# Kernel tuning notes

Hardware: AMD Instinct MI355X
Metric: run time of the kernel (lower is better)

## Reference

```python
import jax, jax.numpy as jnp
import numpy as np

B, S, D_IN, D_OUT, H = 4, 2048, 1024, 1024, 16
HD = D_OUT // H

def setup_inputs() -> dict:
    key = jax.random.key(0)
    ks = jax.random.split(key, 6)
    s = 1.0 / np.sqrt(D_IN)
    return {
        "x": jax.random.normal(ks[0], (B, S, D_IN), dtype=jnp.float32),
        "Wq": jax.random.uniform(ks[1], (D_IN, D_OUT), jnp.float32, -s, s),
        "Wk": jax.random.uniform(ks[2], (D_IN, D_OUT), jnp.float32, -s, s),
        "Wv": jax.random.uniform(ks[3], (D_IN, D_OUT), jnp.float32, -s, s),
        "Wo": jax.random.uniform(ks[4], (D_OUT, D_OUT), jnp.float32, -s, s),
        "bo": jax.random.uniform(ks[5], (D_OUT,), jnp.float32, -s, s),
    }

def reference(x, Wq, Wk, Wv, Wo, bo):
    b, n, _ = x.shape
    # project and split heads: [b, h, n, hd]
    q = (x @ Wq).reshape(b, n, H, HD).transpose(0, 2, 1, 3)
    k = (x @ Wk).reshape(b, n, H, HD).transpose(0, 2, 1, 3)
    v = (x @ Wv).reshape(b, n, H, HD).transpose(0, 2, 1, 3)
    scores = jnp.einsum("bhqd,bhkd->bhqk", q, k) / np.sqrt(HD).astype(np.float32)
    causal = jnp.tril(jnp.ones((n, n), dtype=bool))
    scores = jnp.where(causal, scores, -jnp.inf)
    attn = jax.nn.softmax(scores, axis=-1)  # dropout p=0.0 -> identity
    ctx = jnp.einsum("bhqk,bhkd->bhqd", attn, v)
    ctx = ctx.transpose(0, 2, 1, 3).reshape(b, n, D_OUT)
    return ctx @ Wo + bo
```

## Files before the change

### kernel.cpp

```cpp
#include <hip/hip_runtime.h>
#include <stdint.h>

#define B_   4
#define S_   2048
#define DI   1024
#define DOUT 1024
#define NHD  16
#define HD   64

typedef __attribute__((ext_vector_type(8))) short short8;
typedef __attribute__((ext_vector_type(4))) float f32x4;
typedef __attribute__((ext_vector_type(16))) float f32x16;

__device__ __forceinline__ unsigned short f32_bf16(float f) {
  union { float f; unsigned u; } v; v.f = f;
  unsigned r = v.u + 0x7FFFu + ((v.u >> 16) & 1u);
  return (unsigned short)(r >> 16);
}

__device__ __forceinline__ unsigned pack_bf16x2(float a, float b) {
  union { float f; unsigned u; } x, y; x.f = a; y.f = b;
  return ((y.u + 0x8000u) & 0xFFFF0000u) | ((x.u + 0x8000u) >> 16);
}

__device__ __forceinline__ void gl_lds16(const void* g, void* s) {
  __builtin_amdgcn_global_load_lds(
      (const __attribute__((address_space(1))) unsigned int*)g,
      (__attribute__((address_space(3))) unsigned int*)s, 16, 0, 0);
}

#define EXP2(x) __builtin_amdgcn_exp2f(x)

__global__ __launch_bounds__(256) void cvt_kernel(const float* __restrict__ src,
                                                  unsigned short* __restrict__ dst, int n4) {
  int i = blockIdx.x * blockDim.x + threadIdx.x;
  if (i < n4) {
    float4 v = ((const float4*)src)[i];
    ushort4 o;
    o.x = f32_bf16(v.x); o.y = f32_bf16(v.y); o.z = f32_bf16(v.z); o.w = f32_bf16(v.w);
    ((ushort4*)dst)[i] = o;
  }
}

__global__ __launch_bounds__(256) void wtrans_kernel(const float* __restrict__ W,
                                                     unsigned short* __restrict__ Wt) {
  __shared__ __attribute__((aligned(16))) float tile[64][65];
  const int k0 = blockIdx.y * 64;
  const int n0 = blockIdx.x * 64;
  const int tid = threadIdx.x;
#pragma unroll
  for (int i = 0; i < 4; i++) {
    int c = tid + i * 256;
    int r = c >> 4;
    int cc = (c & 15) * 4;
    float4 v = *(const float4*)(W + (size_t)(k0 + r) * DOUT + n0 + cc);
    tile[r][cc] = v.x; tile[r][cc + 1] = v.y; tile[r][cc + 2] = v.z; tile[r][cc + 3] = v.w;
  }
  __syncthreads();
#pragma unroll
  for (int i = 0; i < 4; i++) {
    int c = tid + i * 256;
    int r = c >> 4;
    int cc = (c & 15) * 4;
    ushort4 o;
    o.x = f32_bf16(tile[cc + 0][r]);
    o.y = f32_bf16(tile[cc + 1][r]);
    o.z = f32_bf16(tile[cc + 2][r]);
    o.w = f32_bf16(tile[cc + 3][r]);
    *(ushort4*)(Wt + (size_t)(n0 + r) * DI + k0 + cc) = o;
  }
}

__global__ __launch_bounds__(256) void vtrans_kernel(const unsigned short* __restrict__ Vb,
                                                     unsigned short* __restrict__ Vt) {
  __shared__ __attribute__((aligned(16))) unsigned short tile[64][72];
  const int bh = blockIdx.y;
  const int s0 = blockIdx.x * 64;
  const int tid = threadIdx.x;
  const unsigned short* src = Vb + (size_t)bh * S_ * HD + (size_t)s0 * HD;
#pragma unroll
  for (int i = 0; i < 2; i++) {
    int c = tid + i * 256;
    int r = c >> 3;
    int cc = (c & 7) * 8;
    *(uint4*)(&tile[r][cc]) = *(const uint4*)(src + r * HD + cc);
  }
  __syncthreads();
  unsigned short* dst = Vt + (size_t)bh * HD * S_ + s0;
#pragma unroll
  for (int i = 0; i < 2; i++) {
    int c = tid + i * 256;
    int r = c >> 3;
    int cc = (c & 7) * 8;
    union { unsigned short u[8]; uint4 v; } t;
#pragma unroll
    for (int j = 0; j < 8; j++) t.u[j] = tile[cc + j][r];
    *(uint4*)(dst + (size_t)r * S_ + cc) = t.v;
  }
}

template <int MODE>
__global__ __launch_bounds__(256) void gemm_kernel(
    const unsigned short* __restrict__ A,
    const unsigned short* __restrict__ Bt,
    unsigned short* __restrict__ oQ,
    unsigned short* __restrict__ oK,
    unsigned short* __restrict__ oV,
    float* __restrict__ outF,
    const float* __restrict__ bias,
    int M, int N, int K) {
  __shared__ __attribute__((aligned(16))) unsigned short Asm_[128 * 32];
  __shared__ __attribute__((aligned(16))) unsigned short Bsm_[128 * 32];
  const int tid = threadIdx.x;
  const int lane = tid & 63;
  const int w = tid >> 6;
  const int wm = w >> 1, wn = w & 1;
  const int quad = lane >> 4, l16 = lane & 15;
  const int m0 = blockIdx.x * 128;
  const int n0 = blockIdx.y * 128;

  const int lr = lane >> 2;
  const int lc8 = (lane & 3) * 8;
  const unsigned short* gA0 = A + (size_t)(m0 + w * 32 + lr) * K + lc8;
  const unsigned short* gA1 = gA0 + (size_t)16 * K;
  const unsigned short* gB0 = Bt + (size_t)(n0 + w * 32 + lr) * K + lc8;
  const unsigned short* gB1 = gB0 + (size_t)16 * K;
  unsigned short* sA0 = Asm_ + (w * 2 + 0) * 512;
  unsigned short* sA1 = Asm_ + (w * 2 + 1) * 512;
  unsigned short* sB0 = Bsm_ + (w * 2 + 0) * 512;
  unsigned short* sB1 = Bsm_ + (w * 2 + 1) * 512;

  f32x4 acc[4][4] = {};

  for (int k0 = 0; k0 < K; k0 += 32) {
    __syncthreads();
    gl_lds16(gA0 + k0, sA0);
    gl_lds16(gA1 + k0, sA1);
    gl_lds16(gB0 + k0, sB0);
    gl_lds16(gB1 + k0, sB1);
    __syncthreads();
    short8 af[4], bfr[4];
#pragma unroll
    for (int mi = 0; mi < 4; mi++)
      af[mi] = *(const short8*)(Asm_ + (wm * 64 + mi * 16 + l16) * 32 + quad * 8);
#pragma unroll
    for (int ni = 0; ni < 4; ni++)
      bfr[ni] = *(const short8*)(Bsm_ + (wn * 64 + ni * 16 + l16) * 32 + quad * 8);
#pragma unroll
    for (int mi = 0; mi < 4; mi++)
#pragma unroll
      for (int ni = 0; ni < 4; ni++)
        acc[mi][ni] = __builtin_amdgcn_mfma_f32_16x16x32_bf16(af[mi], bfr[ni], acc[mi][ni], 0, 0, 0);
  }

  unsigned short* dst0 = nullptr;
  if (MODE == 0) {
    const int which = n0 >> 10;
    dst0 = which == 0 ? oQ : which == 1 ? oK : oV;
  }
#pragma unroll
  for (int mi = 0; mi < 4; mi++) {
#pragma unroll
    for (int ni = 0; ni < 4; ni++) {
      const int col = n0 + wn * 64 + ni * 16 + l16;
      float bv = (MODE == 1) ? bias[col] : 0.f;
#pragma unroll
      for (int r = 0; r < 4; r++) {
        const int row = m0 + wm * 64 + mi * 16 + quad * 4 + r;
        if (MODE == 0) {
          int b = row >> 11, s = row & 2047;
          int h = (col >> 6) & 15, hd = col & 63;
          dst0[(((size_t)(b * NHD + h)) * S_ + s) * HD + hd] = f32_bf16(acc[mi][ni][r]);
        } else {
          outF[(size_t)row * N + col] = acc[mi][ni][r] + bv;
        }
      }
    }
  }
}

__global__ __launch_bounds__(512, 2) void attn_kernel(
    const unsigned short* __restrict__ Q,
    const unsigned short* __restrict__ Kmat,
    const unsigned short* __restrict__ Vt,
    unsigned short* __restrict__ ctx) {
  __shared__ __attribute__((aligned(16))) unsigned short Ks[2][64 * 64];
  __shared__ __attribute__((aligned(16))) unsigned short Vs[2][64 * 64];
  __shared__ __attribute__((aligned(16))) unsigned short PsT[256 * 72];

  const int tid = threadIdx.x;
  const int lane = tid & 63;
  const int w = tid >> 6;
  const int l32 = lane & 31;
  const int h = lane >> 5;

  const int bh = blockIdx.x & 63;
  const int i4 = blockIdx.x >> 6;
  const int jj = (i4 < 4) ? 7 - i4 : i4 - 4;
  const int qc = jj * 8 + w;
  const int nt = (qc >> 1) + 1;
  const int ntmax = jj * 4 + 4;

  const unsigned short* Qh = Q + (size_t)bh * S_ * HD;
  const unsigned short* Kh = Kmat + (size_t)bh * S_ * HD;
  const unsigned short* Vh = Vt + (size_t)bh * HD * S_;

  const int qrow = qc * 32 + l32;

  short8 qf[4];
#pragma unroll
  for (int ks = 0; ks < 4; ks++)
    qf[ks] = *(const short8*)(Qh + (size_t)qrow * HD + ks * 16 + h * 8);

  const int sr = tid >> 3;
  const int sj = tid & 7;
  const int ssw = sr * 64 + ((sj ^ (sr & 7)) << 3);
  const unsigned short* gK = Kh + (size_t)sr * HD + sj * 8;
  const unsigned short* gV = Vh + (size_t)sr * S_ + sj * 8;
  const int swz = (l32 & 7);

  uint4 kreg = *(const uint4*)(gK);
  uint4 vreg = *(const uint4*)(gV);
  *(uint4*)(&Ks[0][ssw]) = kreg;
  *(uint4*)(&Vs[0][ssw]) = vreg;
  __syncthreads();

  f32x16 oacc[2] = {};
  float m_run = -__builtin_inff();
  float l_run = 0.f;
  unsigned short* myP = PsT + (size_t)(w * 32) * 72;
  const float scl = 0.18033688f;

  for (int kt = 0; kt < ntmax; kt++) {
    if (kt + 1 < ntmax) {
      kreg = *(const uint4*)(gK + (size_t)(kt + 1) * 64 * HD);
      vreg = *(const uint4*)(gV + (size_t)(kt + 1) * 64);
    }
    const unsigned short* Kb_ = Ks[kt & 1];
    const unsigned short* Vb_ = Vs[kt & 1];

    if (kt < nt) {
      const int k0 = kt * 64;
      f32x16 sacc[2] = {};
#pragma unroll
      for (int ks = 0; ks < 4; ks++)
#pragma unroll
        for (int mi = 0; mi < 2; mi++) {
          short8 kf = *(const short8*)(Kb_ + (mi * 32 + l32) * 64 + (((ks * 2 + h) ^ swz) << 3));
          sacc[mi] = __builtin_amdgcn_mfma_f32_32x32x16_bf16(kf, qf[ks], sacc[mi], 0, 0, 0);
        }

      if (kt == nt - 1) {
#pragma unroll
        for (int mi = 0; mi < 2; mi++)
#pragma unroll
          for (int e = 0; e < 16; e++) {
            int key = k0 + mi * 32 + (e & 3) + 8 * (e >> 2) + 4 * h;
            if (key > qrow) sacc[mi][e] = -__builtin_inff();
          }
      }
      float vmax = -__builtin_inff();
#pragma unroll
      for (int mi = 0; mi < 2; mi++)
#pragma unroll
        for (int e = 0; e < 16; e++) vmax = fmaxf(vmax, sacc[mi][e]);
      vmax = fmaxf(vmax, __shfl_xor(vmax, 32));
      const float mnew = fmaxf(m_run, vmax * scl);
      const float alpha = EXP2(m_run - mnew);
      m_run = mnew;

      float rs = 0.f;
#pragma unroll
      for (int mi = 0; mi < 2; mi++)
#pragma unroll
        for (int e = 0; e < 16; e++) {
          float p = EXP2(fmaf(sacc[mi][e], scl, -mnew));
          sacc[mi][e] = p;
          rs += p;
        }
      rs += __shfl_xor(rs, 32);
      l_run = l_run * alpha + rs;
#pragma unroll
      for (int mi = 0; mi < 2; mi++) oacc[mi] *= alpha;

#pragma unroll
      for (int mi = 0; mi < 2; mi++)
#pragma unroll
        for (int g = 0; g < 4; g++) {
          uint2 pk;
          pk.x = pack_bf16x2(sacc[mi][4 * g + 0], sacc[mi][4 * g + 1]);
          pk.y = pack_bf16x2(sacc[mi][4 * g + 2], sacc[mi][4 * g + 3]);
          *(uint2*)(myP + l32 * 72 + mi * 32 + g * 8 + h * 4) = pk;
        }

#pragma unroll
      for (int ks2 = 0; ks2 < 4; ks2++) {
        short8 pf = *(const short8*)(myP + l32 * 72 + ks2 * 16 + h * 8);
#pragma unroll
        for (int mi2 = 0; mi2 < 2; mi2++) {
          short8 vf = *(const short8*)(Vb_ + (mi2 * 32 + l32) * 64 + (((ks2 * 2 + h) ^ swz) << 3));
          oacc[mi2] = __builtin_amdgcn_mfma_f32_32x32x16_bf16(vf, pf, oacc[mi2], 0, 0, 0);
        }
      }
    }

    if (kt + 1 < ntmax) {
      *(uint4*)(&Ks[(kt + 1) & 1][ssw]) = kreg;
      *(uint4*)(&Vs[(kt + 1) & 1][ssw]) = vreg;
    }
    __syncthreads();
  }

  const float inv = 1.f / l_run;
#pragma unroll
  for (int mi2 = 0; mi2 < 2; mi2++)
#pragma unroll
    for (int g = 0; g < 4; g++) {
      uint2 pk;
      pk.x = pack_bf16x2(oacc[mi2][4 * g + 0] * inv, oacc[mi2][4 * g + 1] * inv);
      pk.y = pack_bf16x2(oacc[mi2][4 * g + 2] * inv, oacc[mi2][4 * g + 3] * inv);
      *(uint2*)(myP + l32 * 72 + mi2 * 32 + g * 8 + h * 4) = pk;
    }
  const int b = bh >> 4, head = bh & 15;
#pragma unroll
  for (int p = 0; p < 4; p++) {
    int r = p * 8 + (lane >> 3);
    int c = (lane & 7) * 8;
    uint4 vv = *(const uint4*)(myP + r * 72 + c);
    *(uint4*)(ctx + ((size_t)(b * S_ + qc * 32 + r)) * DOUT + head * 64 + c) = vv;
  }
}

extern "C" void kernel_launch(void* const* d_in, const int* in_sizes, int n_in,
                              void* d_out, int out_size, void* d_ws, size_t ws_size,
                              hipStream_t stream) {
  const float* x  = (const float*)d_in[0];
  const float* Wq = (const float*)d_in[1];
  const float* Wk = (const float*)d_in[2];
  const float* Wv = (const float*)d_in[3];
  const float* Wo = (const float*)d_in[4];
  const float* bo = (const float*)d_in[5];
  float* out = (float*)d_out;
  char* ws = (char*)d_ws;

  const size_t MB = 1024 * 1024;
  unsigned short* Wqt = (unsigned short*)(ws + 0 * MB);
  unsigned short* Wkt = (unsigned short*)(ws + 2 * MB);
  unsigned short* Wvt = (unsigned short*)(ws + 4 * MB);
  unsigned short* Wot = (unsigned short*)(ws + 6 * MB);
  unsigned short* xb  = (unsigned short*)(ws + 8 * MB);
  unsigned short* Qb  = (unsigned short*)(ws + 24 * MB);
  unsigned short* Kb  = (unsigned short*)(ws + 40 * MB);
  unsigned short* Vb  = (unsigned short*)(ws + 56 * MB);
  unsigned short* Vtb = (unsigned short*)(ws + 72 * MB);
  unsigned short* ctxb = xb;

  cvt_kernel<<<8192, 256, 0, stream>>>(x, xb, 2097152);
  wtrans_kernel<<<dim3(16, 16), 256, 0, stream>>>(Wq, Wqt);
  wtrans_kernel<<<dim3(16, 16), 256, 0, stream>>>(Wk, Wkt);
  wtrans_kernel<<<dim3(16, 16), 256, 0, stream>>>(Wv, Wvt);
  wtrans_kernel<<<dim3(16, 16), 256, 0, stream>>>(Wo, Wot);
  gemm_kernel<0><<<dim3(64, 24), 256, 0, stream>>>(xb, Wqt, Qb, Kb, Vb, nullptr, nullptr,
                                                   8192, 3072, 1024);
  vtrans_kernel<<<dim3(32, 64), 256, 0, stream>>>(Vb, Vtb);
  attn_kernel<<<512, 512, 0, stream>>>(Qb, Kb, Vtb, ctxb);
  gemm_kernel<1><<<dim3(64, 8), 256, 0, stream>>>(ctxb, Wot, nullptr, nullptr, nullptr, out, bo,
                                                  8192, 1024, 1024);
}
```

Before: 282.5 us.

## Keep P in registers via permlane swaps, lazy rescale, hardware bf16 packing

The attention inner loop now converts probabilities with v_cvt_pk_bf16_f32 and rearranges them into MFMA B-operand layout with v_permlane32_swap, so P no longer goes through an LDS write and read each tile. The online softmax skips rescaling the output accumulator unless the new max exceeds the running max by more than 8 (in log2 units), and the max reduction uses v_max3. The launch-bounds occupancy hint is raised from 2 to 4 blocks per CU, which limits registers per thread. Risks are spills under the tighter register budget, and the fragment remapping must match the MFMA operand layout exactly for results to stay correct.

```diff
diff --git a/kernel.cpp b/kernel.cpp
--- a/kernel.cpp
+++ b/kernel.cpp
@@ -18,9 +18,20 @@
   return (unsigned short)(r >> 16);
 }
 
-__device__ __forceinline__ unsigned pack_bf16x2(float a, float b) {
-  union { float f; unsigned u; } x, y; x.f = a; y.f = b;
-  return ((y.u + 0x8000u) & 0xFFFF0000u) | ((x.u + 0x8000u) >> 16);
+__device__ __forceinline__ unsigned cvt_pk_bf16(float a, float b) {
+  unsigned r;
+  asm("v_cvt_pk_bf16_f32 %0, %1, %2" : "=v"(r) : "v"(a), "v"(b));
+  return r;
+}
+
+__device__ __forceinline__ void pl32swap(unsigned &dst, unsigned &src) {
+  asm("v_permlane32_swap_b32 %0, %1" : "+v"(dst), "+v"(src));
+}
+
+__device__ __forceinline__ float max3f(float a, float b, float c) {
+  float d;
+  asm("v_max3_f32 %0, %1, %2, %3" : "=v"(d) : "v"(a), "v"(b), "v"(c));
+  return d;
 }
 
 __device__ __forceinline__ void gl_lds16(const void* g, void* s) {
@@ -179,7 +190,7 @@
   }
 }
 
-__global__ __launch_bounds__(512, 2) void attn_kernel(
+__global__ __launch_bounds__(512, 4) void attn_kernel(
     const unsigned short* __restrict__ Q,
     const unsigned short* __restrict__ Kmat,
     const unsigned short* __restrict__ Vt,
@@ -259,47 +270,63 @@
             if (key > qrow) sacc[mi][e] = -__builtin_inff();
           }
       }
-      float vmax = -__builtin_inff();
+      float vmax = fmaxf(sacc[0][0], sacc[0][1]);
+#pragma unroll
+      for (int e = 2; e < 16; e += 2) vmax = max3f(vmax, sacc[0][e], sacc[0][e + 1]);
+#pragma unroll
+      for (int e = 0; e < 16; e += 2) vmax = max3f(vmax, sacc[1][e], sacc[1][e + 1]);
+      vmax = fmaxf(vmax, __shfl_xor(vmax, 32));
+      const float pm = vmax * scl;
+      if (!__all(pm <= m_run + 8.f)) {
+        const float mnew = fmaxf(m_run, pm);
+        const float alpha = EXP2(m_run - mnew);
+        m_run = mnew;
+        l_run *= alpha;
+#pragma unroll
+        for (int mi = 0; mi < 2; mi++) oacc[mi] *= alpha;
+      }
+
+      float rs = 0.f;
 #pragma unroll
       for (int mi = 0; mi < 2; mi++)
 #pragma unroll
-        for (int e = 0; e < 16; e++) vmax = fmaxf(vmax, sacc[mi][e]);
-      vmax = fmaxf(vmax, __shfl_xor(vmax, 32));
-      const float mnew = fmaxf(m_run, vmax * scl);
-      const float alpha = EXP2(m_run - mnew);
-      m_run = mnew;
-
-      float rs = 0.f;
-#pragma unroll
-      for (int mi = 0; mi < 2; mi++)
-#pragma unroll
         for (int e = 0; e < 16; e++) {
-          float p = EXP2(fmaf(sacc[mi][e], scl, -mnew));
+          float p = EXP2(fmaf(sacc[mi][e], scl, -m_run));
           sacc[mi][e] = p;
           rs += p;
         }
       rs += __shfl_xor(rs, 32);
-      l_run = l_run * alpha + rs;
-#pragma unroll
-      for (int mi = 0; mi < 2; mi++) oacc[mi] *= alpha;
-
-#pragma unroll
-      for (int mi = 0; mi < 2; mi++)
-#pragma unroll
-        for (int g = 0; g < 4; g++) {
-          uint2 pk;
-          pk.x = pack_bf16x2(sacc[mi][4 * g + 0], sacc[mi][4 * g + 1]);
-          pk.y = pack_bf16x2(sacc[mi][4 * g + 2], sacc[mi][4 * g + 3]);
-          *(uint2*)(myP + l32 * 72 + mi * 32 + g * 8 + h * 4) = pk;
-        }
+      l_run += rs;
+
+      short8 pfr[4];
+#pragma unroll
+      for (int mi = 0; mi < 2; mi++) {
+        unsigned w0 = cvt_pk_bf16(sacc[mi][0], sacc[mi][1]);
+        unsigned w1 = cvt_pk_bf16(sacc[mi][2], sacc[mi][3]);
+        unsigned w2 = cvt_pk_bf16(sacc[mi][4], sacc[mi][5]);
+        unsigned w3 = cvt_pk_bf16(sacc[mi][6], sacc[mi][7]);
+        pl32swap(w0, w2);
+        pl32swap(w1, w3);
+        union { unsigned u[4]; short8 s; } lo;
+        lo.u[0] = w0; lo.u[1] = w1; lo.u[2] = w2; lo.u[3] = w3;
+        pfr[2 * mi + 0] = lo.s;
+        unsigned x0 = cvt_pk_bf16(sacc[mi][8], sacc[mi][9]);
+        unsigned x1 = cvt_pk_bf16(sacc[mi][10], sacc[mi][11]);
+        unsigned x2 = cvt_pk_bf16(sacc[mi][12], sacc[mi][13]);
+        unsigned x3 = cvt_pk_bf16(sacc[mi][14], sacc[mi][15]);
+        pl32swap(x0, x2);
+        pl32swap(x1, x3);
+        union { unsigned u[4]; short8 s; } hi;
+        hi.u[0] = x0; hi.u[1] = x1; hi.u[2] = x2; hi.u[3] = x3;
+        pfr[2 * mi + 1] = hi.s;
+      }
 
 #pragma unroll
       for (int ks2 = 0; ks2 < 4; ks2++) {
-        short8 pf = *(const short8*)(myP + l32 * 72 + ks2 * 16 + h * 8);
 #pragma unroll
         for (int mi2 = 0; mi2 < 2; mi2++) {
           short8 vf = *(const short8*)(Vb_ + (mi2 * 32 + l32) * 64 + (((ks2 * 2 + h) ^ swz) << 3));
-          oacc[mi2] = __builtin_amdgcn_mfma_f32_32x32x16_bf16(vf, pf, oacc[mi2], 0, 0, 0);
+          oacc[mi2] = __builtin_amdgcn_mfma_f32_32x32x16_bf16(vf, pfr[ks2], oacc[mi2], 0, 0, 0);
         }
       }
     }
@@ -317,8 +344,8 @@
 #pragma unroll
     for (int g = 0; g < 4; g++) {
       uint2 pk;
-      pk.x = pack_bf16x2(oacc[mi2][4 * g + 0] * inv, oacc[mi2][4 * g + 1] * inv);
-      pk.y = pack_bf16x2(oacc[mi2][4 * g + 2] * inv, oacc[mi2][4 * g + 3] * inv);
+      pk.x = cvt_pk_bf16(oacc[mi2][4 * g + 0] * inv, oacc[mi2][4 * g + 1] * inv);
+      pk.y = cvt_pk_bf16(oacc[mi2][4 * g + 2] * inv, oacc[mi2][4 * g + 3] * inv);
       *(uint2*)(myP + l32 * 72 + mi2 * 32 + g * 8 + h * 4) = pk;
     }
   const int b = bh >> 4, head = bh & 15;
```

Result: faster. 271.4 us (-3.9%).
